# Performance work log

Measured on AMD Instinct MI355X. Metric: run time of the kernel, lower is better.

## Reference

```python
import jax, jax.numpy as jnp
import numpy as np

B, T, NB = 8192, 18, 6
EH, DH = 256, 256
NIN = NB + 1  # encoder GRU input: bits + feedback scalar


def gru_cell(x, h, Wih, Whh, bih, bhh):
    # PyTorch GRU cell: gates ordered (r, z, n)
    gi = x @ Wih.T + bih
    gh = h @ Whh.T + bhh
    ir, iz, inn = jnp.split(gi, 3, axis=-1)
    hr, hz, hn = jnp.split(gh, 3, axis=-1)
    r = jax.nn.sigmoid(ir + hr)
    z = jax.nn.sigmoid(iz + hz)
    n = jnp.tanh(inn + r * hn)
    return (1.0 - z) * n + z * h


def run_gru_dir(seq, Wih, Whh, bih, bhh, reverse):
    # seq: [T, B, D] -> hidden outputs [T, B, H] (aligned to original time order)
    Bn, H = seq.shape[1], Whh.shape[1]
    def step(h, x):
        h2 = gru_cell(x, h, Wih, Whh, bih, bhh)
        return h2, h2
    _, outs = jax.lax.scan(step, jnp.zeros((Bn, H), seq.dtype), seq, reverse=reverse)
    return outs


def setup_inputs() -> dict:
    key = jax.random.key(0)
    ks = jax.random.split(key, 40)
    def w(k, shape, fan):
        s = 1.0 / np.sqrt(fan)
        return jax.random.uniform(k, shape, jnp.float32, -s, s)
    inp = {}
    inp['b'] = (jax.random.uniform(ks[0], (B, NB)) < 0.5).astype(jnp.float32)
    inp['noise1'] = jax.random.normal(ks[1], (B, T, 1), jnp.float32)
    inp['noise2'] = jax.random.normal(ks[2], (B, T, 1), jnp.float32)
    # encoder GRU (2 layers, unidirectional)
    inp['enc_Wih0'] = w(ks[3], (3 * EH, NIN), EH); inp['enc_Whh0'] = w(ks[4], (3 * EH, EH), EH)
    inp['enc_bih0'] = w(ks[5], (3 * EH,), EH);     inp['enc_bhh0'] = w(ks[6], (3 * EH,), EH)
    inp['enc_Wih1'] = w(ks[7], (3 * EH, EH), EH);  inp['enc_Whh1'] = w(ks[8], (3 * EH, EH), EH)
    inp['enc_bih1'] = w(ks[9], (3 * EH,), EH);     inp['enc_bhh1'] = w(ks[10], (3 * EH,), EH)
    inp['enc_lin_W'] = w(ks[11], (1, EH), EH);     inp['enc_lin_b'] = w(ks[12], (1,), EH)
    inp['weight_power'] = jnp.ones((T,), jnp.float32)
    # decoder GRU (2 layers, bidirectional)
    inp['dec_Wih0f'] = w(ks[13], (3 * DH, 1), DH);      inp['dec_Whh0f'] = w(ks[14], (3 * DH, DH), DH)
    inp['dec_bih0f'] = w(ks[15], (3 * DH,), DH);        inp['dec_bhh0f'] = w(ks[16], (3 * DH,), DH)
    inp['dec_Wih0b'] = w(ks[17], (3 * DH, 1), DH);      inp['dec_Whh0b'] = w(ks[18], (3 * DH, DH), DH)
    inp['dec_bih0b'] = w(ks[19], (3 * DH,), DH);        inp['dec_bhh0b'] = w(ks[20], (3 * DH,), DH)
    inp['dec_Wih1f'] = w(ks[21], (3 * DH, 2 * DH), DH); inp['dec_Whh1f'] = w(ks[22], (3 * DH, DH), DH)
    inp['dec_bih1f'] = w(ks[23], (3 * DH,), DH);        inp['dec_bhh1f'] = w(ks[24], (3 * DH,), DH)
    inp['dec_Wih1b'] = w(ks[25], (3 * DH, 2 * DH), DH); inp['dec_Whh1b'] = w(ks[26], (3 * DH, DH), DH)
    inp['dec_bih1b'] = w(ks[27], (3 * DH,), DH);        inp['dec_bhh1b'] = w(ks[28], (3 * DH,), DH)
    inp['dec_lin_W'] = w(ks[29], (NB, 2 * DH), 2 * DH); inp['dec_lin_b'] = w(ks[30], (NB,), 2 * DH)
    inp['weight_merge'] = jnp.ones((T, 2), jnp.float32)
    return inp


def reference(b, noise1, noise2,
              enc_Wih0, enc_Whh0, enc_bih0, enc_bhh0,
              enc_Wih1, enc_Whh1, enc_bih1, enc_bhh1,
              enc_lin_W, enc_lin_b, weight_power,
              dec_Wih0f, dec_Whh0f, dec_bih0f, dec_bhh0f,
              dec_Wih0b, dec_Whh0b, dec_bih0b, dec_bhh0b,
              dec_Wih1f, dec_Whh1f, dec_bih1f, dec_bhh1f,
              dec_Wih1b, dec_Whh1b, dec_bih1b, dec_bhh1b,
              dec_lin_W, dec_lin_b, weight_merge):
    Bn = b.shape[0]
    Tn = weight_power.shape[0]
    # power-normalized per-step weights: sqrt(w^2 * T / sum(w^2))
    wp = jnp.sqrt(weight_power ** 2 * Tn / jnp.sum(weight_power ** 2))

    def enc_step(carry, xs):
        h0, h1, z = carry
        n1, n2, wpt = xs
        inp = jnp.concatenate([b, z], axis=1)            # [B, NB+1]
        h0n = gru_cell(inp, h0, enc_Wih0, enc_Whh0, enc_bih0, enc_bhh0)
        h1n = gru_cell(h0n, h1, enc_Wih1, enc_Whh1, enc_bih1, enc_bhh1)
        xt = jnp.tanh(h1n @ enc_lin_W.T + enc_lin_b)     # [B, 1]
        xn = (xt - jnp.mean(xt)) / jnp.std(xt, ddof=1)   # training-mode batch norm over whole tensor
        y = xn * wpt + n1                                # received symbol
        return (h0n, h1n, y + n2), y                     # feedback z = y + noise2

    carry0 = (jnp.zeros((Bn, EH), b.dtype), jnp.zeros((Bn, EH), b.dtype), jnp.zeros((Bn, 1), b.dtype))
    xs = (jnp.swapaxes(noise1, 0, 1), jnp.swapaxes(noise2, 0, 1), wp)
    _, y_seq = jax.lax.scan(enc_step, carry0, xs)        # [T, B, 1]

    # bidirectional 2-layer decoder GRU over y
    o0f = run_gru_dir(y_seq, dec_Wih0f, dec_Whh0f, dec_bih0f, dec_bhh0f, False)
    o0b = run_gru_dir(y_seq, dec_Wih0b, dec_Whh0b, dec_bih0b, dec_bhh0b, True)
    s1 = jnp.concatenate([o0f, o0b], axis=-1)            # [T, B, 2*DH]
    o1f = run_gru_dir(s1, dec_Wih1f, dec_Whh1f, dec_bih1f, dec_bhh1f, False)
    o1b = run_gru_dir(s1, dec_Wih1b, dec_Whh1b, dec_bih1b, dec_bhh1b, True)

    # attention_type == 5: learned weighted merge over time, per direction
    wf = jnp.sqrt(weight_merge[:, 0] ** 2 * Tn / jnp.sum(weight_merge[:, 0] ** 2))
    wb = jnp.sqrt(weight_merge[:, 1] ** 2 * Tn / jnp.sum(weight_merge[:, 1] ** 2))
    rf = jnp.einsum('tbh,t->bh', o1f, wf)
    rb = jnp.einsum('tbh,t->bh', o1b, wb)
    rc = jnp.concatenate([rf, rb], axis=1)               # [B, 2*DH]
    out = jax.nn.sigmoid(rc @ dec_lin_W.T + dec_lin_b)   # bit_vector output -> sigmoid
    return out.reshape(Bn, -1, 1)
```

## Files before the change

kernel.cpp:

```cpp
#include <hip/hip_runtime.h>
#include <hip/hip_bf16.h>
#include <math.h>

#define BN_ 8192
#define TT 18
#define NBITS 6
#define HH 256
#define G3 768

typedef __hip_bfloat16 hbf16;
typedef __bf16 bf16x8 __attribute__((ext_vector_type(8)));
typedef float f32x4 __attribute__((ext_vector_type(4)));

__device__ inline float sigm(float x){ return 1.0f/(1.0f + expf(-x)); }
__device__ inline float ldx(const void* p, int i, int bf){
    if(bf){ unsigned short u = ((const unsigned short*)p)[i]; return __uint_as_float(((unsigned)u)<<16); }
    return ((const float*)p)[i];
}
__device__ inline __bf16 f2b(float f){ hbf16 h = __float2bfloat16(f); return *reinterpret_cast<__bf16*>(&h); }
__device__ inline float b2f(__bf16 b){ unsigned short u = *reinterpret_cast<unsigned short*>(&b); return __uint_as_float(((unsigned)u)<<16); }
__device__ inline unsigned pack2(float a, float b){
    hbf16 lo = __float2bfloat16(a), hi = __float2bfloat16(b);
    return (unsigned)*(unsigned short*)&lo | ((unsigned)*(unsigned short*)&hi << 16);
}

__global__ __launch_bounds__(256) void fillz(float* __restrict__ p, int n){
    for(int i = blockIdx.x*256 + threadIdx.x; i < n; i += gridDim.x*256) p[i] = 0.0f;
}
__global__ __launch_bounds__(256) void fillb(__bf16* __restrict__ p, int n){
    for(int i = blockIdx.x*256 + threadIdx.x; i < n; i += gridDim.x*256) p[i] = f2b(0.0f);
}

__global__ void prep_w(const void* wp, const void* wm, unsigned* flag,
                       float* wpn, float* wfn, float* wbn){
    if(threadIdx.x==0 && blockIdx.x==0){
        unsigned w0 = *(const unsigned*)wp;
        int bf = ((w0 >> 16) == (w0 & 0xFFFFu)) ? 1 : 0;
        flag[0] = (unsigned)bf;
        float s=0; for(int t=0;t<TT;t++){ float v=ldx(wp,t,bf); s += v*v; }
        for(int t=0;t<TT;t++){ float v=ldx(wp,t,bf); wpn[t] = sqrtf(v*v*TT/s); }
        float sf=0, sb=0;
        for(int t=0;t<TT;t++){ float f=ldx(wm,2*t,bf), b=ldx(wm,2*t+1,bf); sf += f*f; sb += b*b; }
        for(int t=0;t<TT;t++){
            float f=ldx(wm,2*t,bf), b=ldx(wm,2*t+1,bf);
            wfn[t] = sqrtf(f*f*TT/sf);
            wbn[t] = sqrtf(b*b*TT/sb);
        }
    }
}

struct CJ { const void* src; void* dst; int n; int K; int mode; };
struct CJs { CJ j[20]; };
__global__ __launch_bounds__(256) void conv_all(CJs J, const unsigned* __restrict__ flagp){
    const int bf = (int)*flagp;
    CJ c = J.j[blockIdx.y];
    for(int i = blockIdx.x*256 + threadIdx.x; i < c.n; i += gridDim.x*256){
        if(c.mode==1){
            int row = i / c.K, k = i - row*c.K;
            int g = row>>8, jj = row&255;
            int prow = ((jj>>4)*48) + g*16 + (jj&15);
            ((__bf16*)c.dst)[(size_t)prow*c.K + k] = f2b(ldx(c.src, i, bf));
        }else if(c.mode==2){
            int t = i >> 13, b = i & (BN_-1);
            ((float*)c.dst)[i] = ldx(c.src, b*TT + t, bf);
        }else{
            ((float*)c.dst)[i] = ldx(c.src, i, bf);
        }
    }
}

struct FQ {
    const __bf16* A1; const __bf16* W1; int K1;
    const __bf16* A2; const __bf16* W2; int K2;
    const float* bgi; const float* bgh;
    const __bf16* h; __bf16* hout;
    const void* bits; const void* wih0raw; const void* bih0raw; const float* zf;
    const void* linw; float* xt;
    const float* y; const void* wihraw; const void* bihraw; __bf16* s1t;
    float* racc; const float* wct;
};
struct FQ2 { FQ q[2]; };

template<int MODE>
__global__ __launch_bounds__(256,3) void fused_step(FQ2 PP, const unsigned* __restrict__ flagp){
    const FQ P = PP.q[blockIdx.z];
    const int bf = (int)*flagp;
    __shared__ __align__(16) char smem[28672];
    __bf16* As = (__bf16*)smem;
    __bf16* Ws = (__bf16*)(smem + 16384);
    float*  T  = (float*)smem;
    const int tid = threadIdx.x;
    const int mt = blockIdx.x*8 + (blockIdx.y>>3);
    const int jt = blockIdx.y & 7;
    const int m0 = mt*128;
    const int n0 = jt*96;
    const int lane = tid&63, wv = tid>>6;
    const int wrow = wv>>1, wcol = wv&1;
    const int q = lane>>4, n15 = lane&15;

    f32x4 accR[4], accZ[4], accN1[4], accN2[4];
    #pragma unroll
    for(int i=0;i<4;i++){ accR[i]=(f32x4){0,0,0,0}; accZ[i]=(f32x4){0,0,0,0};
                          accN1[i]=(f32x4){0,0,0,0}; accN2[i]=(f32x4){0,0,0,0}; }

    #pragma unroll
    for(int ph = 0; ph < 2; ph++){
        if(ph==0 && !(MODE==1 || MODE==3)) continue;
        const __bf16* __restrict__ A = ph ? P.A2 : P.A1;
        const __bf16* __restrict__ W = ph ? P.W2 : P.W1;
        const int K = ph ? P.K2 : P.K1;
        for(int k0=0;k0<K;k0+=64){
            #pragma unroll
            for(int s=0;s<4;s++){
                int c = tid + 256*s;
                int row = c>>3, qc = c&7, col = qc ^ ((row>>1)&7);
                *(uint4*)&As[row*64 + col*8] = *(const uint4*)(A + (size_t)(m0+row)*K + k0 + qc*8);
            }
            #pragma unroll
            for(int s=0;s<3;s++){
                int c = tid + 256*s;
                int row = c>>3, qc = c&7, col = qc ^ ((row>>1)&7);
                *(uint4*)&Ws[row*64 + col*8] = *(const uint4*)(W + (size_t)(n0+row)*K + k0 + qc*8);
            }
            __syncthreads();
            #pragma unroll
            for(int ks=0;ks<2;ks++){
                const int cq = ks*4 + q;
                bf16x8 af[4], bfr[3];
                #pragma unroll
                for(int i=0;i<4;i++){
                    int R = wrow*64+i*16+n15;
                    int col = cq ^ ((R>>1)&7);
                    af[i] = *(const bf16x8*)&As[R*64 + col*8];
                }
                #pragma unroll
                for(int g=0;g<3;g++){
                    int RW = wcol*48+g*16+n15;
                    int col = cq ^ ((RW>>1)&7);
                    bfr[g] = *(const bf16x8*)&Ws[RW*64 + col*8];
                }
                #pragma unroll
                for(int i=0;i<4;i++){
                    accR[i] = __builtin_amdgcn_mfma_f32_16x16x32_bf16(af[i], bfr[0], accR[i], 0,0,0);
                    accZ[i] = __builtin_amdgcn_mfma_f32_16x16x32_bf16(af[i], bfr[1], accZ[i], 0,0,0);
                    if(ph) accN2[i] = __builtin_amdgcn_mfma_f32_16x16x32_bf16(af[i], bfr[2], accN2[i], 0,0,0);
                    else   accN1[i] = __builtin_amdgcn_mfma_f32_16x16x32_bf16(af[i], bfr[2], accN1[i], 0,0,0);
                }
            }
            __syncthreads();
        }
    }

    const int jl = wcol*16 + n15;
    const int j  = jt*32 + jl;
    const float bghr = P.bgh[j], bghz = P.bgh[256+j], bghn = P.bgh[512+j];
    float bgir=0, bgiz=0, bgin=0;
    if(MODE==1 || MODE==3){ bgir = P.bgi[j]; bgiz = P.bgi[256+j]; bgin = P.bgi[512+j]; }
    float w0r[7], w0z[7], w0n[7];
    if(MODE==0){
        #pragma unroll
        for(int k=0;k<7;k++){
            w0r[k] = ldx(P.wih0raw, (j    )*7+k, bf);
            w0z[k] = ldx(P.wih0raw, (j+256)*7+k, bf);
            w0n[k] = ldx(P.wih0raw, (j+512)*7+k, bf);
        }
        bgir = ldx(P.bih0raw, j, bf); bgiz = ldx(P.bih0raw, j+256, bf); bgin = ldx(P.bih0raw, j+512, bf);
    }
    float wy_r=0, wy_z=0, wy_n=0;
    if(MODE==2){
        wy_r = ldx(P.wihraw, j, bf); wy_z = ldx(P.wihraw, j+256, bf); wy_n = ldx(P.wihraw, j+512, bf);
        bgir = ldx(P.bihraw, j, bf); bgiz = ldx(P.bihraw, j+256, bf); bgin = ldx(P.bihraw, j+512, bf);
    }
    const float linwj = (MODE==1) ? ldx(P.linw, j, bf) : 0.0f;
    const float wct   = (MODE==3) ? P.wct[0] : 0.0f;

    #pragma unroll
    for(int i=0;i<4;i++){
        const int rbl = wrow*64 + i*16 + q*4;
        float vred[4];
        #pragma unroll
        for(int r=0;r<4;r++){
            const int row_l = rbl + r;
            const int row = m0 + row_l;
            float gir, giz, gin;
            if(MODE==1 || MODE==3){
                gir = bgir; giz = bgiz; gin = accN1[i][r] + bgin;
            }else if(MODE==0){
                gir = bgir; giz = bgiz; gin = bgin;
                #pragma unroll
                for(int k=0;k<NBITS;k++){
                    float bv = ldx(P.bits, row*NBITS+k, bf);
                    gir += bv*w0r[k]; giz += bv*w0z[k]; gin += bv*w0n[k];
                }
                float zb = P.zf[row];
                gir += zb*w0r[6]; giz += zb*w0z[6]; gin += zb*w0n[6];
            }else{
                float yv = P.y[row];
                gir = yv*wy_r + bgir; giz = yv*wy_z + bgiz; gin = yv*wy_n + bgin;
            }
            float rr = sigm(gir + accR[i][r] + bghr);
            float zz = sigm(giz + accZ[i][r] + bghz);
            float nn = tanhf(gin + rr*(accN2[i][r] + bghn));
            float hold = b2f(P.h[(size_t)row*HH + j]);
            float hn = (1.0f - zz)*nn + zz*hold;
            T[row_l*33 + jl] = hn;
            if(MODE==1) vred[r] = hn*linwj;
        }
        if(MODE==1){
            #pragma unroll
            for(int r=0;r<4;r++){
                float v = vred[r];
                #pragma unroll
                for(int m=1;m<16;m<<=1) v += __shfl_xor(v, m);
                if(n15==0) atomicAdd(&P.xt[m0+rbl+r], v);
            }
        }
    }
    __syncthreads();

    const int rw2 = tid>>2, cw = tid&3;
    #pragma unroll
    for(int pass=0; pass<2; pass++){
        const int row_l = pass*64 + rw2;
        const int row = m0 + row_l;
        float v[8];
        #pragma unroll
        for(int u=0;u<8;u++) v[u] = T[row_l*33 + cw*8 + u];
        uint4 pkv = { pack2(v[0],v[1]), pack2(v[2],v[3]), pack2(v[4],v[5]), pack2(v[6],v[7]) };
        *(uint4*)&P.hout[(size_t)row*HH + jt*32 + cw*8] = pkv;
        if(MODE==2) *(uint4*)&P.s1t[(size_t)row*512 + jt*32 + cw*8] = pkv;
        if(MODE==3){
            float* rp = &P.racc[(size_t)row*HH + jt*32 + cw*8];
            float4 a0 = *(float4*)rp, a1 = *(float4*)(rp+4);
            a0.x += wct*v[0]; a0.y += wct*v[1]; a0.z += wct*v[2]; a0.w += wct*v[3];
            a1.x += wct*v[4]; a1.y += wct*v[5]; a1.z += wct*v[6]; a1.w += wct*v[7];
            *(float4*)rp = a0; *(float4*)(rp+4) = a1;
        }
    }
}

__global__ __launch_bounds__(1024) void stats_emit(float* __restrict__ xt, const void* __restrict__ lb,
        const float* __restrict__ wpn, int t, const float* __restrict__ n1t, const float* __restrict__ n2t,
        float* __restrict__ yseq, float* __restrict__ zf, const unsigned* __restrict__ flagp){
    const int bf = (int)*flagp;
    const float lbv = ldx(lb, 0, bf);
    int tid = threadIdx.x;
    float s=0.0f, ss=0.0f;
    for(int i=tid;i<BN_;i+=1024){ float v = tanhf(xt[i] + lbv); s += v; ss += v*v; }
    #pragma unroll
    for(int o=32;o;o>>=1){ s += __shfl_down(s,o); ss += __shfl_down(ss,o); }
    __shared__ float S[16], SS[16], stm[2];
    if((tid&63)==0){ S[tid>>6]=s; SS[tid>>6]=ss; }
    __syncthreads();
    if(tid==0){
        float a=0.0f, b=0.0f;
        for(int i=0;i<16;i++){ a+=S[i]; b+=SS[i]; }
        float mean = a/(float)BN_;
        float var = (b - (float)BN_*mean*mean)/(float)(BN_-1);
        stm[0]=mean; stm[1]=1.0f/sqrtf(var);
    }
    __syncthreads();
    const float mean=stm[0], rs=stm[1], wt=wpn[t];
    for(int i=tid;i<BN_;i+=1024){
        float v = tanhf(xt[i] + lbv);
        float y = (v-mean)*rs*wt + n1t[i];
        yseq[(size_t)t*BN_ + i] = y;
        zf[i] = y + n2t[i];
        xt[i] = 0.0f;
    }
}

__global__ __launch_bounds__(256) void final_k(const float* __restrict__ rf, const float* __restrict__ rb,
        const void* __restrict__ W, const void* __restrict__ bias, void* __restrict__ out,
        const unsigned* __restrict__ flagp){
    const int bf = (int)*flagp;
    int lane = threadIdx.x & 63;
    int row = blockIdx.x*4 + (threadIdx.x>>6);
    float a[6] = {};
    #pragma unroll
    for(int i=0;i<4;i++){
        int c = lane + 64*i;
        float xf = rf[(size_t)row*HH + c];
        float xb = rb[(size_t)row*HH + c];
        #pragma unroll
        for(int k=0;k<6;k++) a[k] += xf*ldx(W, k*512 + c, bf) + xb*ldx(W, k*512 + 256 + c, bf);
    }
    #pragma unroll
    for(int o=32;o;o>>=1){
        #pragma unroll
        for(int k=0;k<6;k++) a[k] += __shfl_down(a[k], o);
    }
    if(lane==0){
        #pragma unroll
        for(int k=0;k<6;k++){
            float v = sigm(a[k] + ldx(bias,k,bf));
            if(bf) ((hbf16*)out)[(size_t)row*6+k] = __float2bfloat16(v);
            else   ((float*)out)[(size_t)row*6+k] = v;
        }
    }
}

extern "C" void kernel_launch(void* const* d_in, const int* in_sizes, int n_in,
                              void* d_out, int out_size, void* d_ws, size_t ws_size,
                              hipStream_t stream)
{
    (void)in_sizes; (void)n_in; (void)out_size;
    const void* bits  = d_in[0];
    const void* n1    = d_in[1];
    const void* n2    = d_in[2];
    const void* eWih0 = d_in[3];
    const void* eWhh0 = d_in[4];
    const void* ebih0 = d_in[5];
    const void* ebhh0 = d_in[6];
    const void* eWih1 = d_in[7];
    const void* eWhh1 = d_in[8];
    const void* ebih1 = d_in[9];
    const void* ebhh1 = d_in[10];
    const void* elinW = d_in[11];
    const void* elinb = d_in[12];
    const void* wpow  = d_in[13];
    const void* dWih0f= d_in[14];
    const void* dWhh0f= d_in[15];
    const void* dbih0f= d_in[16];
    const void* dbhh0f= d_in[17];
    const void* dWih0b= d_in[18];
    const void* dWhh0b= d_in[19];
    const void* dbih0b= d_in[20];
    const void* dbhh0b= d_in[21];
    const void* dWih1f= d_in[22];
    const void* dWhh1f= d_in[23];
    const void* dbih1f= d_in[24];
    const void* dbhh1f= d_in[25];
    const void* dWih1b= d_in[26];
    const void* dWhh1b= d_in[27];
    const void* dbih1b= d_in[28];
    const void* dbhh1b= d_in[29];
    const void* dlinW = d_in[30];
    const void* dlinb = d_in[31];
    const void* wmrg  = d_in[32];

    float* base = (float*)d_ws;
    size_t off = 0;
    auto alloc  = [&](size_t n){ float* p = base + off; off += (n + 63) & ~(size_t)63; return p; };
    auto allocb = [&](size_t n){ __bf16* p = (__bf16*)(base + off); off += ((n/2) + 63) & ~(size_t)63; return p; };
    unsigned* flag = (unsigned*)alloc(64);
    float* wpn = alloc(TT); float* wfn = alloc(TT); float* wbn = alloc(TT);
    const int WK = HH*G3;
    __bf16* WeHH0 = allocb(WK);  __bf16* WeIH1 = allocb(WK);  __bf16* WeHH1 = allocb(WK);
    __bf16* Wd0f  = allocb(WK);  __bf16* Wd0b  = allocb(WK);
    __bf16* Wd1fI = allocb(2*WK);__bf16* Wd1bI = allocb(2*WK);
    __bf16* Wd1fH = allocb(WK);  __bf16* Wd1bH = allocb(WK);
    float* BeHH0 = alloc(G3); float* BeIH1 = alloc(G3); float* BeHH1 = alloc(G3);
    float* Bd0f  = alloc(G3); float* Bd0b  = alloc(G3);
    float* Bd1fI = alloc(G3); float* Bd1bI = alloc(G3);
    float* Bd1fH = alloc(G3); float* Bd1bH = alloc(G3);
    const size_t NH = (size_t)BN_*HH;
    __bf16* X0 = allocb(NH);  __bf16* X1 = allocb(NH);
    __bf16* Y0 = allocb(NH);  __bf16* Y1 = allocb(NH);
    float* rf  = alloc(NH);
    float* rb  = alloc(NH);
    float* xt  = alloc(BN_);
    float* zf  = alloc(BN_);
    float* yseq= alloc((size_t)TT*BN_);
    float* n1t = alloc((size_t)TT*BN_);
    float* n2t = alloc((size_t)TT*BN_);
    __bf16* s1 = allocb((size_t)TT*BN_*512);
    size_t need = off*sizeof(float);
    if(ws_size < need) return;

    prep_w<<<1,64,0,stream>>>(wpow, wmrg, flag, wpn, wfn, wbn);
    CJs J;
    const void* ws_src[20] = {eWhh0,eWih1,eWhh1,dWhh0f,dWhh0b,dWih1f,dWih1b,dWhh1f,dWhh1b,
                              ebhh0,ebih1,ebhh1,dbhh0f,dbhh0b,dbih1f,dbih1b,dbhh1f,dbhh1b, n1, n2};
    void* ws_dst[20] = {WeHH0,WeIH1,WeHH1,Wd0f,Wd0b,Wd1fI,Wd1bI,Wd1fH,Wd1bH,
                        BeHH0,BeIH1,BeHH1,Bd0f,Bd0b,Bd1fI,Bd1bI,Bd1fH,Bd1bH, n1t, n2t};
    int ws_n[20] = {WK,WK,WK,WK,WK,2*WK,2*WK,WK,WK, G3,G3,G3,G3,G3,G3,G3,G3,G3, TT*BN_, TT*BN_};
    int ws_K[20] = {256,256,256,256,256,512,512,256,256, 0,0,0,0,0,0,0,0,0, 0,0};
    int ws_m[20] = {1,1,1,1,1,1,1,1,1, 0,0,0,0,0,0,0,0,0, 2,2};
    for(int i=0;i<20;i++){ J.j[i] = {ws_src[i], ws_dst[i], ws_n[i], ws_K[i], ws_m[i]}; }
    conv_all<<<dim3(768,20),256,0,stream>>>(J, flag);
    fillb<<<1024,256,0,stream>>>(X0, (int)NH);
    fillb<<<1024,256,0,stream>>>(Y0, (int)NH);
    fillz<<<32,256,0,stream>>>(xt, BN_);
    fillz<<<32,256,0,stream>>>(zf, BN_);

    dim3 g1(8, 64, 1), g2(8, 64, 2);
    __bf16* X[2] = {X0, X1};
    __bf16* Y[2] = {Y0, Y1};

    int p = 0;
    for(int t=0;t<TT;t++){
        FQ2 P0{}; FQ2 P1{};
        FQ& a = P0.q[0];
        a.A2=X[p]; a.W2=WeHH0; a.K2=HH; a.bgh=BeHH0; a.h=X[p]; a.hout=X[1-p];
        a.bits=bits; a.wih0raw=eWih0; a.bih0raw=ebih0; a.zf=zf;
        fused_step<0><<<g1,256,0,stream>>>(P0, flag);
        FQ& b = P1.q[0];
        b.A1=X[1-p]; b.W1=WeIH1; b.K1=HH; b.A2=Y[p]; b.W2=WeHH1; b.K2=HH;
        b.bgi=BeIH1; b.bgh=BeHH1; b.h=Y[p]; b.hout=Y[1-p];
        b.linw=elinW; b.xt=xt;
        fused_step<1><<<g1,256,0,stream>>>(P1, flag);
        stats_emit<<<1,1024,0,stream>>>(xt, elinb, wpn, t, n1t+(size_t)t*BN_, n2t+(size_t)t*BN_,
                                        yseq, zf, flag);
        p ^= 1;
    }

    fillb<<<1024,256,0,stream>>>(X0, (int)NH);
    fillb<<<1024,256,0,stream>>>(Y0, (int)NH);
    p = 0;
    for(int i=0;i<TT;i++){
        int tf = i, tb = TT-1-i;
        FQ2 P{};
        FQ& a = P.q[0];
        a.A2=X[p]; a.W2=Wd0f; a.K2=HH; a.bgh=Bd0f; a.h=X[p]; a.hout=X[1-p];
        a.y=yseq+(size_t)tf*BN_; a.wihraw=dWih0f; a.bihraw=dbih0f; a.s1t=s1+(size_t)tf*BN_*512;
        FQ& b = P.q[1];
        b.A2=Y[p]; b.W2=Wd0b; b.K2=HH; b.bgh=Bd0b; b.h=Y[p]; b.hout=Y[1-p];
        b.y=yseq+(size_t)tb*BN_; b.wihraw=dWih0b; b.bihraw=dbih0b; b.s1t=s1+(size_t)tb*BN_*512+256;
        fused_step<2><<<g2,256,0,stream>>>(P, flag);
        p ^= 1;
    }

    fillb<<<1024,256,0,stream>>>(X0, (int)NH);
    fillb<<<1024,256,0,stream>>>(Y0, (int)NH);
    fillz<<<1024,256,0,stream>>>(rf, (int)(2*NH));
    p = 0;
    for(int i=0;i<TT;i++){
        int tf = i, tb = TT-1-i;
        FQ2 P{};
        FQ& a = P.q[0];
        a.A1=s1+(size_t)tf*BN_*512; a.W1=Wd1fI; a.K1=512;
        a.A2=X[p]; a.W2=Wd1fH; a.K2=HH; a.bgi=Bd1fI; a.bgh=Bd1fH; a.h=X[p]; a.hout=X[1-p];
        a.racc=rf; a.wct=wfn+tf;
        FQ& b = P.q[1];
        b.A1=s1+(size_t)tb*BN_*512; b.W1=Wd1bI; b.K1=512;
        b.A2=Y[p]; b.W2=Wd1bH; b.K2=HH; b.bgi=Bd1bI; b.bgh=Bd1bH; b.h=Y[p]; b.hout=Y[1-p];
        b.racc=rb; b.wct=wbn+tb;
        fused_step<3><<<g2,256,0,stream>>>(P, flag);
        p ^= 1;
    }

    final_k<<<BN_/4,256,0,stream>>>(rf, rb, dlinW, dlinb, d_out, flag);
}
```

Before: 1.890 ms.

## Pipeline decoder layer-1 input projection one step ahead of recurrent GEMM

Splits the layer-1 decoder step into two jobs: an input-projection GEMM (K=512) that writes gate pre-activations to a bf16 buffer, and a recurrent GEMM (K=256) that reads them. Each launch now does the recurrence for step t alongside the input projection for step t+1, so the two run in one 4-way grid instead of one serial K=768 pass per block. This shortens the per-block dependency chain and raises occupancy per launch. The cost is extra global traffic for the double-buffered gate tensors, and the input gates are rounded to bf16, which adds precision loss.

```diff
diff --git a/kernel.cpp b/kernel.cpp
--- a/kernel.cpp
+++ b/kernel.cpp
@@ -77,7 +77,6 @@
     const void* bits; const void* wih0raw; const void* bih0raw; const float* zf;
     const void* linw; float* xt;
     const float* y; const void* wihraw; const void* bihraw; __bf16* s1t;
-    float* racc; const float* wct;
 };
 struct FQ2 { FQ q[2]; };
 
@@ -105,7 +104,7 @@
 
     #pragma unroll
     for(int ph = 0; ph < 2; ph++){
-        if(ph==0 && !(MODE==1 || MODE==3)) continue;
+        if(ph==0 && MODE!=1) continue;
         const __bf16* __restrict__ A = ph ? P.A2 : P.A1;
         const __bf16* __restrict__ W = ph ? P.W2 : P.W1;
         const int K = ph ? P.K2 : P.K1;
@@ -155,7 +154,7 @@
     const int j  = jt*32 + jl;
     const float bghr = P.bgh[j], bghz = P.bgh[256+j], bghn = P.bgh[512+j];
     float bgir=0, bgiz=0, bgin=0;
-    if(MODE==1 || MODE==3){ bgir = P.bgi[j]; bgiz = P.bgi[256+j]; bgin = P.bgi[512+j]; }
+    if(MODE==1){ bgir = P.bgi[j]; bgiz = P.bgi[256+j]; bgin = P.bgi[512+j]; }
     float w0r[7], w0z[7], w0n[7];
     if(MODE==0){
         #pragma unroll
@@ -172,7 +171,6 @@
         bgir = ldx(P.bihraw, j, bf); bgiz = ldx(P.bihraw, j+256, bf); bgin = ldx(P.bihraw, j+512, bf);
     }
     const float linwj = (MODE==1) ? ldx(P.linw, j, bf) : 0.0f;
-    const float wct   = (MODE==3) ? P.wct[0] : 0.0f;
 
     #pragma unroll
     for(int i=0;i<4;i++){
@@ -183,7 +181,7 @@
             const int row_l = rbl + r;
             const int row = m0 + row_l;
             float gir, giz, gin;
-            if(MODE==1 || MODE==3){
+            if(MODE==1){
                 gir = bgir; giz = bgiz; gin = accN1[i][r] + bgin;
             }else if(MODE==0){
                 gir = bgir; giz = bgiz; gin = bgin;
@@ -229,8 +227,138 @@
         uint4 pkv = { pack2(v[0],v[1]), pack2(v[2],v[3]), pack2(v[4],v[5]), pack2(v[6],v[7]) };
         *(uint4*)&P.hout[(size_t)row*HH + jt*32 + cw*8] = pkv;
         if(MODE==2) *(uint4*)&P.s1t[(size_t)row*512 + jt*32 + cw*8] = pkv;
-        if(MODE==3){
-            float* rp = &P.racc[(size_t)row*HH + jt*32 + cw*8];
+    }
+}
+
+struct MJ {
+    int mode; int K;
+    const __bf16* A; const __bf16* W; const float* bias;
+    __bf16* gout;
+    const __bf16* gin;
+    const __bf16* h; __bf16* hout; float* racc; const float* wct;
+};
+struct MJ4 { MJ j[4]; };
+
+__global__ __launch_bounds__(256,3) void fused_mix(MJ4 PP){
+    const MJ J = PP.j[blockIdx.z];
+    __shared__ __align__(16) char smem[28672];
+    __bf16* As = (__bf16*)smem;
+    __bf16* Ws = (__bf16*)(smem + 16384);
+    float*  T  = (float*)smem;
+    const int tid = threadIdx.x;
+    const int mt = blockIdx.x*8 + (blockIdx.y>>3);
+    const int jt = blockIdx.y & 7;
+    const int m0 = mt*128, n0 = jt*96;
+    const int lane = tid&63, wv = tid>>6;
+    const int wrow = wv>>1, wcol = wv&1;
+    const int q = lane>>4, n15 = lane&15;
+
+    f32x4 acc[3][4];
+    #pragma unroll
+    for(int g=0;g<3;g++)
+        #pragma unroll
+        for(int i=0;i<4;i++) acc[g][i]=(f32x4){0,0,0,0};
+
+    const __bf16* __restrict__ A = J.A;
+    const __bf16* __restrict__ W = J.W;
+    const int K = J.K;
+    for(int k0=0;k0<K;k0+=64){
+        #pragma unroll
+        for(int s=0;s<4;s++){
+            int c = tid + 256*s;
+            int row = c>>3, qc = c&7, col = qc ^ ((row>>1)&7);
+            *(uint4*)&As[row*64 + col*8] = *(const uint4*)(A + (size_t)(m0+row)*K + k0 + qc*8);
+        }
+        #pragma unroll
+        for(int s=0;s<3;s++){
+            int c = tid + 256*s;
+            int row = c>>3, qc = c&7, col = qc ^ ((row>>1)&7);
+            *(uint4*)&Ws[row*64 + col*8] = *(const uint4*)(W + (size_t)(n0+row)*K + k0 + qc*8);
+        }
+        __syncthreads();
+        #pragma unroll
+        for(int ks=0;ks<2;ks++){
+            const int cq = ks*4 + q;
+            bf16x8 af[4], bfr[3];
+            #pragma unroll
+            for(int i=0;i<4;i++){
+                int R = wrow*64+i*16+n15;
+                int col = cq ^ ((R>>1)&7);
+                af[i] = *(const bf16x8*)&As[R*64 + col*8];
+            }
+            #pragma unroll
+            for(int g=0;g<3;g++){
+                int RW = wcol*48+g*16+n15;
+                int col = cq ^ ((RW>>1)&7);
+                bfr[g] = *(const bf16x8*)&Ws[RW*64 + col*8];
+            }
+            #pragma unroll
+            for(int i=0;i<4;i++){
+                acc[0][i] = __builtin_amdgcn_mfma_f32_16x16x32_bf16(af[i], bfr[0], acc[0][i], 0,0,0);
+                acc[1][i] = __builtin_amdgcn_mfma_f32_16x16x32_bf16(af[i], bfr[1], acc[1][i], 0,0,0);
+                acc[2][i] = __builtin_amdgcn_mfma_f32_16x16x32_bf16(af[i], bfr[2], acc[2][i], 0,0,0);
+            }
+        }
+        __syncthreads();
+    }
+
+    const int jl = wcol*16 + n15;
+    const int j  = jt*32 + jl;
+    const float bg0 = J.bias[j], bg1 = J.bias[256+j], bg2 = J.bias[512+j];
+    const int rw2 = tid>>2, cw = tid&3;
+
+    if(J.mode==4){
+        const float bgs[3] = {bg0, bg1, bg2};
+        for(int g=0; g<3; g++){
+            if(g) __syncthreads();
+            #pragma unroll
+            for(int i=0;i<4;i++){
+                const int rbl = wrow*64 + i*16 + q*4;
+                #pragma unroll
+                for(int r=0;r<4;r++) T[(rbl+r)*33 + jl] = acc[g][i][r] + bgs[g];
+            }
+            __syncthreads();
+            #pragma unroll
+            for(int pass=0; pass<2; pass++){
+                const int row_l = pass*64 + rw2;
+                const int row = m0 + row_l;
+                float v[8];
+                #pragma unroll
+                for(int u=0;u<8;u++) v[u] = T[row_l*33 + cw*8 + u];
+                uint4 pkv = { pack2(v[0],v[1]), pack2(v[2],v[3]), pack2(v[4],v[5]), pack2(v[6],v[7]) };
+                *(uint4*)&J.gout[(size_t)row*G3 + jt*96 + g*32 + cw*8] = pkv;
+            }
+        }
+    }else{
+        #pragma unroll
+        for(int i=0;i<4;i++){
+            const int rbl = wrow*64 + i*16 + q*4;
+            #pragma unroll
+            for(int r=0;r<4;r++){
+                const int row_l = rbl + r;
+                const int row = m0 + row_l;
+                const __bf16* gb = J.gin + (size_t)row*G3 + jt*96;
+                float gir = b2f(gb[jl]), giz = b2f(gb[32+jl]), gnn = b2f(gb[64+jl]);
+                float rr = sigm(gir + acc[0][i][r] + bg0);
+                float zz = sigm(giz + acc[1][i][r] + bg1);
+                float nn = tanhf(gnn + rr*(acc[2][i][r] + bg2));
+                float hold = b2f(J.h[(size_t)row*HH + j]);
+                float hn = (1.0f - zz)*nn + zz*hold;
+                T[row_l*33 + jl] = hn;
+            }
+        }
+        __syncthreads();
+        const float wct = J.wct[0];
+        #pragma unroll
+        for(int pass=0; pass<2; pass++){
+            const int row_l = pass*64 + rw2;
+            const int row = m0 + row_l;
+            float v[8];
+            #pragma unroll
+            for(int u=0;u<8;u++) v[u] = T[row_l*33 + cw*8 + u];
+            uint4 pkv = { pack2(v[0],v[1]), pack2(v[2],v[3]), pack2(v[4],v[5]), pack2(v[6],v[7]) };
+            *(uint4*)&J.hout[(size_t)row*HH + jt*32 + cw*8] = pkv;
+            float* rp = &J.racc[(size_t)row*HH + jt*32 + cw*8];
             float4 a0 = *(float4*)rp, a1 = *(float4*)(rp+4);
             a0.x += wct*v[0]; a0.y += wct*v[1]; a0.z += wct*v[2]; a0.w += wct*v[3];
             a1.x += wct*v[4]; a1.y += wct*v[5]; a1.z += wct*v[6]; a1.w += wct*v[7];
@@ -364,6 +492,8 @@
     float* yseq= alloc((size_t)TT*BN_);
     float* n1t = alloc((size_t)TT*BN_);
     float* n2t = alloc((size_t)TT*BN_);
+    __bf16* giF0 = allocb((size_t)BN_*G3);  __bf16* giF1 = allocb((size_t)BN_*G3);
+    __bf16* giB0 = allocb((size_t)BN_*G3);  __bf16* giB1 = allocb((size_t)BN_*G3);
     __bf16* s1 = allocb((size_t)TT*BN_*512);
     size_t need = off*sizeof(float);
     if(ws_size < need) return;
@@ -384,9 +514,11 @@
     fillz<<<32,256,0,stream>>>(xt, BN_);
     fillz<<<32,256,0,stream>>>(zf, BN_);
 
-    dim3 g1(8, 64, 1), g2(8, 64, 2);
+    dim3 g1(8, 64, 1), g2(8, 64, 2), g4(8, 64, 4);
     __bf16* X[2] = {X0, X1};
     __bf16* Y[2] = {Y0, Y1};
+    __bf16* giF[2] = {giF0, giF1};
+    __bf16* giB[2] = {giB0, giB1};
 
     int p = 0;
     for(int t=0;t<TT;t++){
@@ -424,19 +556,27 @@
     fillb<<<1024,256,0,stream>>>(X0, (int)NH);
     fillb<<<1024,256,0,stream>>>(Y0, (int)NH);
     fillz<<<1024,256,0,stream>>>(rf, (int)(2*NH));
+    {
+        MJ4 P{};
+        P.j[0] = {4, 512, s1, Wd1fI, Bd1fI, giF[0], nullptr, nullptr, nullptr, nullptr, nullptr};
+        P.j[1] = {4, 512, s1+(size_t)(TT-1)*BN_*512, Wd1bI, Bd1bI, giB[0], nullptr, nullptr, nullptr, nullptr, nullptr};
+        fused_mix<<<g2,256,0,stream>>>(P);
+    }
     p = 0;
     for(int i=0;i<TT;i++){
         int tf = i, tb = TT-1-i;
-        FQ2 P{};
-        FQ& a = P.q[0];
-        a.A1=s1+(size_t)tf*BN_*512; a.W1=Wd1fI; a.K1=512;
-        a.A2=X[p]; a.W2=Wd1fH; a.K2=HH; a.bgi=Bd1fI; a.bgh=Bd1fH; a.h=X[p]; a.hout=X[1-p];
-        a.racc=rf; a.wct=wfn+tf;
-        FQ& b = P.q[1];
-        b.A1=s1+(size_t)tb*BN_*512; b.W1=Wd1bI; b.K1=512;
-        b.A2=Y[p]; b.W2=Wd1bH; b.K2=HH; b.bgi=Bd1bI; b.bgh=Bd1bH; b.h=Y[p]; b.hout=Y[1-p];
-        b.racc=rb; b.wct=wbn+tb;
-        fused_step<3><<<g2,256,0,stream>>>(P, flag);
+        MJ4 P{};
+        P.j[0] = {5, 256, X[p], Wd1fH, Bd1fH, nullptr, giF[i&1], X[p], X[1-p], rf, wfn+tf};
+        P.j[1] = {5, 256, Y[p], Wd1bH, Bd1bH, nullptr, giB[i&1], Y[p], Y[1-p], rb, wbn+tb};
+        if(i < TT-1){
+            P.j[2] = {4, 512, s1+(size_t)(tf+1)*BN_*512, Wd1fI, Bd1fI, giF[(i+1)&1],
+                      nullptr, nullptr, nullptr, nullptr, nullptr};
+            P.j[3] = {4, 512, s1+(size_t)(tb-1)*BN_*512, Wd1bI, Bd1bI, giB[(i+1)&1],
+                      nullptr, nullptr, nullptr, nullptr, nullptr};
+            fused_mix<<<g4,256,0,stream>>>(P);
+        }else{
+            fused_mix<<<g2,256,0,stream>>>(P);
+        }
         p ^= 1;
     }
 
```

Result: slower. 1.995 ms (+5.6%).
